# Optimization experiments

Measured on AMD Instinct MI355X. Metric: run time of the kernel, lower is better.

## Reference

```python
import jax, jax.numpy as jnp
import numpy as np
import math

# Static problem sizes (match init_kwargs: dims=(32,32) -> m = 64 modes).
D = 32            # dims[0] == dims[1]
M = 2 * D         # number of optical modes
B = 16            # batch size of density matrices
# Fock basis for 2 photons in M modes (bunching allowed): pairs (j, k), j <= k.
JJ, KK = np.triu_indices(M)          # each length F = M*(M+1)//2 = 2080
BUNCHED = (JJ == KK)                 # states with both photons in the same mode


def setup_inputs() -> dict:
    key = jax.random.key(0)
    k0, k1, k2, k3 = jax.random.split(key, 4)
    rho_re = jax.random.normal(k0, (B, D * D, D * D), dtype=jnp.float32)
    rho_im = jax.random.normal(k1, (B, D * D, D * D), dtype=jnp.float32)
    # Stand-in for the interferometer unitary produced from phi; scaled ~1/sqrt(M)
    U_re = jax.random.normal(k2, (M, M), dtype=jnp.float32) / math.sqrt(M)
    U_im = jax.random.normal(k3, (M, M), dtype=jnp.float32) / math.sqrt(M)
    return {"rho_re": rho_re, "rho_im": rho_im, "U_re": U_re, "U_im": U_im}


def _slos_amplitudes(U):
    """2-photon SLOS amplitudes for all d^2 one-hot input pairs.

    Input state (x, y): photons in modes p = x and q = D + y (distinct modes,
    so input norm factor is 1).  Output amplitude for Fock state with photons
    in modes (j, k), j <= k, is perm(U[{j,k},{p,q}]) / sqrt(n_out!):
        j < k : U[j,p]U[k,q] + U[k,p]U[j,q]
        j = k : 2 U[j,p]U[j,q] / sqrt(2)
    Returns amplitudes of shape [D*D, F] with (x, y) flattened x-major,
    matching the original input_states loop order.
    """
    Up = U[:, :D]   # columns for photon 1 modes p = x,      shape [M, D]
    Uq = U[:, D:]   # columns for photon 2 modes q = D + y,  shape [M, D]
    jj = jnp.asarray(JJ)
    kk = jnp.asarray(KK)
    # amp[x, y, f] = Up[jj[f], x] * Uq[kk[f], y] + Up[kk[f], x] * Uq[jj[f], y]
    amp = (jnp.einsum('fx,fy->xyf', Up[jj], Uq[kk])
           + jnp.einsum('fx,fy->xyf', Up[kk], Uq[jj]))
    scale = jnp.where(jnp.asarray(BUNCHED), 1.0 / math.sqrt(2.0), 1.0)
    amp = amp * scale.astype(amp.real.dtype)
    return amp.reshape(D * D, -1)   # [D*D, F]


def reference(rho_re, rho_im, U_re, U_im):
    U = jax.lax.complex(U_re, U_im)                  # [M, M] complex64
    rho = jax.lax.complex(rho_re, rho_im)            # [B, D^2, D^2] complex64

    amplitudes = _slos_amplitudes(U)                 # [D^2, F]
    u_evolve = amplitudes.T                          # [F, D^2]
    u_evolve_dag = jnp.conj(u_evolve)                # conj; transpose handled in einsum

    # upper-triangular part of rho with the diagonal halved
    upper = jnp.triu(rho)
    eye = jnp.eye(D * D, dtype=bool)
    upper = jnp.where(eye, upper * 0.5, upper)

    # inter = U_ev @ upper @ U_ev^dagger   (batched over B)
    tmp = jnp.einsum('fi,bij->bfj', u_evolve, upper)         # [B, F, D^2]
    inter = jnp.einsum('bfj,gj->bfg', tmp, u_evolve_dag)     # [B, F, F]

    new_rho = inter + jnp.conj(jnp.swapaxes(inter, 1, 2))    # Hermitian result
    # return real/imag stacked on last axis to keep dtypes real
    return jnp.stack([new_rho.real, new_rho.imag], axis=-1)  # [B, F, F, 2]
```

## Files before the change

### kernel.cpp

```cpp
#include <hip/hip_runtime.h>

#define NBATCH 16
#define NK     1024
#define MMODES 64
#define FOUT   2080
#define FPAD   2176
#define TILEM  128
#define TILEN  64
#define BK     32

typedef __attribute__((ext_vector_type(8))) short bf16x8;
typedef __attribute__((ext_vector_type(4))) float f32x4;
typedef __attribute__((ext_vector_type(4))) unsigned int u32x4;

__device__ __forceinline__ unsigned short f2bf(float f) {
  union { float f; unsigned u; } v; v.f = f;
  unsigned r = v.u + 0x7fffu + ((v.u >> 16) & 1u);
  return (unsigned short)(r >> 16);
}

__device__ __forceinline__ void gl2lds16(const unsigned short* g, unsigned short* l) {
  __builtin_amdgcn_global_load_lds((const __attribute__((address_space(1))) void*)g,
                                   (__attribute__((address_space(3))) void*)l, 16, 0, 0);
}

__device__ __forceinline__ void stage_tile(const unsigned short* gbase, unsigned short* lds,
                                           int tid, int halves) {
  int lane = tid & 63;
  int wv   = tid >> 6;
  int rIn  = lane >> 2;
  int kOfs = (lane & 3) << 3;
#pragma unroll
  for (int it = 0; it < halves; ++it) {
    int chunk = wv + (it << 2);
    int row = (chunk << 4) + rIn;
    gl2lds16(gbase + (size_t)row * NK + kOfs, lds + (chunk << 9));
  }
}

__device__ __forceinline__ bf16x8 negbf8(bf16x8 x) {
  u32x4 t = *(const u32x4*)&x;
  t ^= 0x80008000u;
  return *(const bf16x8*)&t;
}

__global__ __launch_bounds__(256, 3)
void cgemm(const unsigned short* __restrict__ Are0, const unsigned short* __restrict__ Aim0, long aB,
           const unsigned short* __restrict__ Bre0, const unsigned short* __restrict__ Bim0, long bB,
           unsigned short* Tre0, unsigned short* Tim0, long tB,
           float* out0, long oB, int mode)
{
  __shared__ __align__(16) unsigned short sAre[TILEM * BK];
  __shared__ __align__(16) unsigned short sAim[TILEM * BK];
  __shared__ __align__(16) unsigned short sBre[TILEN * BK];
  __shared__ __align__(16) unsigned short sBim[TILEN * BK];

  const int tid  = threadIdx.x;
  const int z    = blockIdx.z;
  const int bm   = blockIdx.y;
  const int bn   = blockIdx.x;
  const int lane = tid & 63;
  const int wv   = tid >> 6;
  const int wm   = wv >> 1;
  const int wn   = wv & 1;
  const int quad = lane >> 4;
  const int lcol = lane & 15;

  const unsigned short* Are = Are0 + (size_t)z * aB;
  const unsigned short* Aim = Aim0 + (size_t)z * aB;
  const unsigned short* Bre = Bre0 + (size_t)z * bB;
  const unsigned short* Bim = Bim0 + (size_t)z * bB;

  f32x4 accRe[4][2], accIm[4][2];
#pragma unroll
  for (int mt = 0; mt < 4; ++mt)
#pragma unroll
    for (int nt = 0; nt < 2; ++nt) {
      accRe[mt][nt] = (f32x4){0.f, 0.f, 0.f, 0.f};
      accIm[mt][nt] = (f32x4){0.f, 0.f, 0.f, 0.f};
    }

  const unsigned short* gAre = Are + (size_t)(bm * TILEM) * NK;
  const unsigned short* gAim = Aim + (size_t)(bm * TILEM) * NK;
  const unsigned short* gBre = Bre + (size_t)(bn * TILEN) * NK;
  const unsigned short* gBim = Bim + (size_t)(bn * TILEN) * NK;

  const int aOff = (wm * 64 + lcol) * BK + quad * 8;
  const int bOff = (wn * 32 + lcol) * BK + quad * 8;

  for (int kt = 0; kt < NK / BK; ++kt) {
    __syncthreads();
    const int k0 = kt * BK;
    stage_tile(gAre + k0, sAre, tid, 2);
    stage_tile(gAim + k0, sAim, tid, 2);
    stage_tile(gBre + k0, sBre, tid, 1);
    stage_tile(gBim + k0, sBim, tid, 1);
    __syncthreads();

    bf16x8 ar[4], ai[4], br[2], bi[2], bn_[2];
#pragma unroll
    for (int mt = 0; mt < 4; ++mt) {
      ar[mt] = *(const bf16x8*)(sAre + aOff + mt * 16 * BK);
      ai[mt] = *(const bf16x8*)(sAim + aOff + mt * 16 * BK);
    }
#pragma unroll
    for (int nt = 0; nt < 2; ++nt) {
      br[nt] = *(const bf16x8*)(sBre + bOff + nt * 16 * BK);
      bi[nt] = *(const bf16x8*)(sBim + bOff + nt * 16 * BK);
      bn_[nt] = negbf8(bi[nt]);
    }
#pragma unroll
    for (int mt = 0; mt < 4; ++mt)
#pragma unroll
      for (int nt = 0; nt < 2; ++nt) {
        accRe[mt][nt] = __builtin_amdgcn_mfma_f32_16x16x32_bf16(ar[mt], br[nt],  accRe[mt][nt], 0, 0, 0);
        accRe[mt][nt] = __builtin_amdgcn_mfma_f32_16x16x32_bf16(ai[mt], bn_[nt], accRe[mt][nt], 0, 0, 0);
        accIm[mt][nt] = __builtin_amdgcn_mfma_f32_16x16x32_bf16(ar[mt], bi[nt],  accIm[mt][nt], 0, 0, 0);
        accIm[mt][nt] = __builtin_amdgcn_mfma_f32_16x16x32_bf16(ai[mt], br[nt],  accIm[mt][nt], 0, 0, 0);
      }
  }

  if (mode == 1) {
    unsigned short* Tre = Tre0 + (size_t)z * tB;
    unsigned short* Tim = Tim0 + (size_t)z * tB;
#pragma unroll
    for (int mt = 0; mt < 4; ++mt)
#pragma unroll
      for (int nt = 0; nt < 2; ++nt) {
        const int col = bn * TILEN + wn * 32 + nt * 16 + lcol;
        const int fb  = bm * TILEM + wm * 64 + mt * 16 + quad * 4;
#pragma unroll
        for (int r = 0; r < 4; ++r) {
          Tre[(size_t)(fb + r) * NK + col] = f2bf(accRe[mt][nt][r]);
          Tim[(size_t)(fb + r) * NK + col] = f2bf(-accIm[mt][nt][r]);
        }
      }
  } else {
    float* out = out0 + (size_t)z * oB;
#pragma unroll
    for (int mt = 0; mt < 4; ++mt)
#pragma unroll
      for (int nt = 0; nt < 2; ++nt) {
        const int g  = bn * TILEN + wn * 32 + nt * 16 + lcol;
        const int fb = bm * TILEM + wm * 64 + mt * 16 + quad * 4;
#pragma unroll
        for (int r = 0; r < 4; ++r) {
          const int f = fb + r;
          if (f < FOUT && g < FOUT) {
            float2 v;
            v.x = accRe[mt][nt][r];
            v.y = -accIm[mt][nt][r];
            *(float2*)(out + ((size_t)f * FOUT + g) * 2) = v;
          }
        }
      }
  }
}

__global__ void prepA(const float* __restrict__ Ure, const float* __restrict__ Uim,
                      unsigned short* __restrict__ Are, unsigned short* __restrict__ Aim)
{
  const int f  = blockIdx.x;
  const int i0 = threadIdx.x * 4;
  const size_t base = (size_t)f * NK + i0;
  if (f >= FOUT) {
#pragma unroll
    for (int r = 0; r < 4; ++r) { Are[base + r] = 0; Aim[base + r] = 0; }
    return;
  }
  int fr = f, j = 0;
  while (fr >= MMODES - j) { fr -= MMODES - j; ++j; }
  const int k = j + fr;
  const float s = (j == k) ? 0.70710678118654752f : 1.0f;
  const int x = i0 >> 5;
  const float ujxr = Ure[j * MMODES + x], ujxi = Uim[j * MMODES + x];
  const float ukxr = Ure[k * MMODES + x], ukxi = Uim[k * MMODES + x];
#pragma unroll
  for (int r = 0; r < 4; ++r) {
    const int y = (i0 + r) & 31;
    const float ukyr = Ure[k * MMODES + 32 + y], ukyi = Uim[k * MMODES + 32 + y];
    const float ujyr = Ure[j * MMODES + 32 + y], ujyi = Uim[j * MMODES + 32 + y];
    float re = ujxr * ukyr - ujxi * ukyi + ukxr * ujyr - ukxi * ujyi;
    float im = ujxr * ukyi + ujxi * ukyr + ukxr * ujyi + ukxi * ujyr;
    Are[base + r] = f2bf(s * re);
    Aim[base + r] = f2bf(s * im);
  }
}

__global__ void prepH(const float* __restrict__ rho_re, const float* __restrict__ rho_im,
                      unsigned short* __restrict__ Htre, unsigned short* __restrict__ Htim, int b0)
{
  const int z = blockIdx.z;
  const size_t rbase = (size_t)(b0 + z) * NK * NK;
  const int lin = blockIdx.x * blockDim.x + threadIdx.x;
  const int j = lin >> 10, i = lin & 1023;
  const int lo = min(i, j), hi = max(i, j);
  const size_t src = rbase + (size_t)lo * NK + hi;
  const float re = rho_re[src];
  const float im = (i < j) ? rho_im[src] : (i > j) ? -rho_im[src] : 0.f;
  const size_t o = (size_t)z * NK * NK + lin;
  Htre[o] = f2bf(re);
  Htim[o] = f2bf(im);
}

extern "C" void kernel_launch(void* const* d_in, const int* in_sizes, int n_in,
                              void* d_out, int out_size, void* d_ws, size_t ws_size,
                              hipStream_t stream) {
  const float* rho_re = (const float*)d_in[0];
  const float* rho_im = (const float*)d_in[1];
  const float* U_re   = (const float*)d_in[2];
  const float* U_im   = (const float*)d_in[3];
  float* out = (float*)d_out;

  char* ws = (char*)d_ws;
  const size_t szA = (size_t)FPAD * NK * 2;
  unsigned short* Are  = (unsigned short*)(ws);
  unsigned short* Aim  = (unsigned short*)(ws + szA);
  const size_t oHt = 2 * szA;
  const size_t szH = (size_t)2 * NK * NK * 2;
  unsigned short* Htre = (unsigned short*)(ws + oHt);
  unsigned short* Htim = (unsigned short*)(ws + oHt + szH);
  const size_t oT = oHt + 2 * szH;
  const size_t szT = (size_t)2 * FPAD * NK * 2;
  unsigned short* Tre  = (unsigned short*)(ws + oT);
  unsigned short* Tim  = (unsigned short*)(ws + oT + szT);

  prepA<<<dim3(FPAD, 1, 1), dim3(256), 0, stream>>>(U_re, U_im, Are, Aim);

  for (int p = 0; p < 8; ++p) {
    prepH<<<dim3(4096, 1, 2), dim3(256), 0, stream>>>(rho_re, rho_im, Htre, Htim, p * 2);
    cgemm<<<dim3(16, 17, 2), dim3(256), 0, stream>>>(
        Are, Aim, 0L, Htre, Htim, (long)NK * NK,
        Tre, Tim, (long)FPAD * NK, (float*)nullptr, 0L, 1);
    cgemm<<<dim3(33, 17, 2), dim3(256), 0, stream>>>(
        Tre, Tim, (long)FPAD * NK, Are, Aim, 0L,
        (unsigned short*)nullptr, (unsigned short*)nullptr, 0L,
        out + (size_t)p * 2 * FOUT * FOUT * 2, (long)FOUT * FOUT * 2, 2);
  }
}
```

Before: 1.818 ms.

## Exploit Hermitian symmetry: compute upper output tiles only, mirror via conjugate transpose

The second complex GEMM now exits early for output tiles that lie entirely below the diagonal, roughly halving that GEMM's work. A new hermitize kernel afterwards fills the lower triangle of each batch's output by conjugate-transposing the upper tiles through shared memory. This adds an extra memory pass over the output in exchange for the saved matrix-multiply work.

```diff
diff --git a/kernel.cpp b/kernel.cpp
--- a/kernel.cpp
+++ b/kernel.cpp
@@ -59,6 +59,9 @@
   const int z    = blockIdx.z;
   const int bm   = blockIdx.y;
   const int bn   = blockIdx.x;
+
+  if (mode == 2 && bn < 2 * bm) return;
+
   const int lane = tid & 63;
   const int wv   = tid >> 6;
   const int wm   = wv >> 1;
@@ -154,6 +157,49 @@
           }
         }
       }
+  }
+}
+
+#define HT 32
+#define NTILE 65
+__global__ __launch_bounds__(256)
+void hermitize(float* __restrict__ out0)
+{
+  __shared__ float2 ld[HT][HT + 1];
+  const int tid = threadIdx.x;
+  const int t = blockIdx.x;
+  int tr = (int)((sqrtf(8.f * (float)t + 1.f) - 1.f) * 0.5f);
+  if (tr < 0) tr = 0;
+  if (tr > NTILE - 1) tr = NTILE - 1;
+  while (tr + 1 <= NTILE - 1 && (tr + 1) * (tr + 2) / 2 <= t) ++tr;
+  while (tr > 0 && tr * (tr + 1) / 2 > t) --tr;
+  const int tc = t - tr * (tr + 1) / 2;
+
+  float* out = out0 + (size_t)blockIdx.z * FOUT * FOUT * 2;
+
+  const int gj = tid & 31;
+  const int i4 = (tid >> 5) << 2;
+#pragma unroll
+  for (int r = 0; r < 4; ++r) {
+    const int fi = i4 + r;
+    const int f = tc * HT + fi;
+    const int g = tr * HT + gj;
+    float2 v = *(const float2*)(out + ((size_t)f * FOUT + g) * 2);
+    ld[gj][fi] = v;
+  }
+  __syncthreads();
+
+  const int fi2 = tid & 31;
+  const int j4 = (tid >> 5) << 2;
+#pragma unroll
+  for (int r = 0; r < 4; ++r) {
+    const int j = j4 + r;
+    if (tr == tc && j <= fi2) continue;
+    float2 v = ld[j][fi2];
+    v.y = -v.y;
+    const int grow = tr * HT + j;
+    const int fcol = tc * HT + fi2;
+    *(float2*)(out + ((size_t)grow * FOUT + fcol) * 2) = v;
   }
 }
 
@@ -237,4 +283,6 @@
         (unsigned short*)nullptr, (unsigned short*)nullptr, 0L,
         out + (size_t)p * 2 * FOUT * FOUT * 2, (long)FOUT * FOUT * 2, 2);
   }
-}
+
+  hermitize<<<dim3(NTILE * (NTILE + 1) / 2, 1, NBATCH), dim3(256), 0, stream>>>(out);
+}
```

Measured after the change: 1.608 ms. -11.5%, faster.
